# Optimization experiments

Hardware: AMD Instinct MI355X
Metric: run time of the kernel (lower is better)

## Reference

```python
import jax, jax.numpy as jnp
import numpy as np

LN_EPS = 1e-5
NUM_HEAD = 8


def _layernorm(x, gamma, beta):
    mu = jnp.mean(x, axis=-1, keepdims=True)
    var = jnp.var(x, axis=-1, keepdims=True)
    return (x - mu) * jax.lax.rsqrt(var + LN_EPS) * gamma + beta


def setup_inputs() -> dict:
    key = jax.random.key(0)
    ks = jax.random.split(key, 5)
    b, T, N, C = 16, 256, 24, 512
    scale = 1.0 / np.sqrt(C)
    return {
        "x": jax.random.normal(ks[0], (b, T, N, C), dtype=jnp.float32),
        "cross_x": jax.random.normal(ks[1], (b, T, N, C), dtype=jnp.float32),
        "gamma": jnp.ones((C,), dtype=jnp.float32),
        "beta": jnp.zeros((C,), dtype=jnp.float32),
        "Wq": (jax.random.normal(ks[2], (C, C), dtype=jnp.float32) * scale),
        "Wk": (jax.random.normal(ks[3], (C, C), dtype=jnp.float32) * scale),
        "Wv": (jax.random.normal(ks[4], (C, C), dtype=jnp.float32) * scale),
    }


def reference(x, cross_x, gamma, beta, Wq, Wk, Wv):
    b, T, N, C = x.shape
    H = NUM_HEAD
    d = C // H
    # fold joints into batch: (b, T, N, C) -> (b*N, T, C)
    xr = jnp.transpose(x, (0, 2, 1, 3)).reshape(b * N, T, C)
    cr = jnp.transpose(cross_x, (0, 2, 1, 3)).reshape(b * N, T, C)
    B = b * N
    xn = _layernorm(xr, gamma, beta)
    cn = _layernorm(cr, gamma, beta)
    # nn.Linear: y = x @ W.T (weight stored [out, in])
    q = jnp.einsum('btc,oc->bto', xn, Wq).reshape(B, T, H, d)
    k = jnp.einsum('btc,oc->bto', cn, Wk).reshape(B, T, H, d)
    v = jnp.einsum('btc,oc->bto', cn, Wv).reshape(B, T, H, d)
    att = jnp.einsum('bnhd,bmhd->bnmh', q, k) / np.sqrt(d).astype(np.float32)
    w = jax.nn.softmax(att, axis=2)  # softmax over key axis m (dropout=0)
    y = jnp.einsum('bnmh,bmhd->bnhd', w, v).reshape(B, T, C)
    y = xr + y
    return jnp.transpose(y.reshape(b, N, T, C), (0, 2, 1, 3))
```

## Files before the change

### kernel.cpp

```cpp
#include <hip/hip_runtime.h>

typedef __bf16 bf16x8 __attribute__((ext_vector_type(8)));
typedef float f32x4 __attribute__((ext_vector_type(4)));

#define MFMA16(a, b, c) __builtin_amdgcn_mfma_f32_16x16x32_bf16(a, b, c, 0, 0, 0)

__device__ __forceinline__ void gload_lds16(const void* g, void* l) {
  __builtin_amdgcn_global_load_lds(
      (const __attribute__((address_space(1))) void*)(unsigned long long)g,
      (__attribute__((address_space(3))) void*)(unsigned int)(unsigned long long)l,
      16, 0, 0);
}

__global__ void cvt_w_kernel(const float* __restrict__ wq, const float* __restrict__ wk,
                             const float* __restrict__ wv, __bf16* __restrict__ w) {
  int i = blockIdx.x * 256 + threadIdx.x;
  w[i]          = (__bf16)wq[i];
  w[i + 262144] = (__bf16)wk[i];
  w[i + 524288] = (__bf16)wv[i];
}

__global__ __launch_bounds__(256) void ln_kernel(
    const float* __restrict__ x, const float* __restrict__ cx,
    const float* __restrict__ g, const float* __restrict__ bet,
    __bf16* __restrict__ xn) {
  int wave = threadIdx.x >> 6, lane = threadIdx.x & 63;
  long row = (long)blockIdx.x * 4 + wave;
  const float* src = (row < 98304) ? (x + row * 512) : (cx + (row - 98304) * 512);
  const f32x4* p = (const f32x4*)(src + lane * 8);
  f32x4 a = p[0], b = p[1];
  float s  = a[0] + a[1] + a[2] + a[3] + b[0] + b[1] + b[2] + b[3];
  float s2 = a[0]*a[0] + a[1]*a[1] + a[2]*a[2] + a[3]*a[3]
           + b[0]*b[0] + b[1]*b[1] + b[2]*b[2] + b[3]*b[3];
  for (int d = 1; d < 64; d <<= 1) { s += __shfl_xor(s, d, 64); s2 += __shfl_xor(s2, d, 64); }
  float mean = s * (1.0f / 512.0f);
  float var  = s2 * (1.0f / 512.0f) - mean * mean;
  float rs = rsqrtf(var + 1e-5f);
  const f32x4* gp = (const f32x4*)(g + lane * 8);
  const f32x4* bp = (const f32x4*)(bet + lane * 8);
  f32x4 g0 = gp[0], g1 = gp[1], b0 = bp[0], b1 = bp[1];
  bf16x8 o;
  for (int j = 0; j < 4; ++j) o[j]     = (__bf16)((a[j] - mean) * rs * g0[j] + b0[j]);
  for (int j = 0; j < 4; ++j) o[4 + j] = (__bf16)((b[j] - mean) * rs * g1[j] + b1[j]);
  *(bf16x8*)(xn + row * 512 + lane * 8) = o;
}

__global__ __launch_bounds__(256) void gemm_qkv_kernel(
    const __bf16* __restrict__ act, const __bf16* __restrict__ w,
    __bf16* __restrict__ outqkv) {
  int z = blockIdx.z;
  const __bf16* A = act + (z ? (long)50331648 : 0);
  const __bf16* B = w + (long)z * 262144;
  __bf16* C = outqkv + (long)z * 50331648;
  int m0 = blockIdx.x * 128, n0 = blockIdx.y * 128;
  int tid = threadIdx.x, wave = tid >> 6, lane = tid & 63;
  int q4 = lane >> 4, cl = lane & 15;
  int wm = wave & 1, wn = wave >> 1;
  __shared__ __bf16 As[128 * 64];
  __shared__ __bf16 Bs[128 * 64];
  f32x4 acc[4][4] = {};
  for (int kb = 0; kb < 512; kb += 64) {
    for (int i = 0; i < 4; ++i) {
      int t = i * 256 + tid;
      int row = t >> 3;
      int col = (t & 7) * 8;
      gload_lds16(A + (long)(m0 + row) * 512 + kb + col, (char*)As + (i * 256 + wave * 64) * 16);
      gload_lds16(B + (long)(n0 + row) * 512 + kb + col, (char*)Bs + (i * 256 + wave * 64) * 16);
    }
    __syncthreads();
    for (int kc = 0; kc < 2; ++kc) {
      bf16x8 af[4], bfr[4];
      for (int mt = 0; mt < 4; ++mt)
        af[mt] = *(const bf16x8*)(As + (wm * 64 + mt * 16 + cl) * 64 + kc * 32 + q4 * 8);
      for (int nt = 0; nt < 4; ++nt)
        bfr[nt] = *(const bf16x8*)(Bs + (wn * 64 + nt * 16 + cl) * 64 + kc * 32 + q4 * 8);
      for (int mt = 0; mt < 4; ++mt)
        for (int nt = 0; nt < 4; ++nt)
          acc[mt][nt] = MFMA16(af[mt], bfr[nt], acc[mt][nt]);
    }
    __syncthreads();
  }
  for (int mt = 0; mt < 4; ++mt)
    for (int nt = 0; nt < 4; ++nt) {
      int row = m0 + wm * 64 + mt * 16 + q4 * 4;
      int col = n0 + wn * 64 + nt * 16 + cl;
      for (int r = 0; r < 4; ++r)
        C[(long)(row + r) * 512 + col] = (__bf16)acc[mt][nt][r];
    }
}

__global__ __launch_bounds__(256) void attn_kernel(
    const __bf16* __restrict__ Q, const __bf16* __restrict__ K,
    const __bf16* __restrict__ V, const float* __restrict__ x,
    float* __restrict__ out) {
  int blk = blockIdx.x;
  int h = blk & 7;
  int rem = blk >> 3;
  int n_ = rem % 24;
  int b_ = rem / 24;
  long base = ((long)b_ * 6144 + n_) * 512 + h * 64;
  const long ST = 12288;
  int tid = threadIdx.x, wave = tid >> 6, lane = tid & 63;
  int q4 = lane >> 4, cl = lane & 15;
  __shared__ __bf16 Vt[64][264];
  __shared__ __bf16 Pb[4][16][72];

  {
    const __bf16* vrow = V + base + (long)tid * ST;
    for (int i = 0; i < 8; ++i) {
      bf16x8 v = *(const bf16x8*)(vrow + i * 8);
      for (int j = 0; j < 8; ++j) Vt[i * 8 + j][tid] = v[j];
    }
  }
  __syncthreads();

  for (int iter = 0; iter < 4; ++iter) {
    int mt = iter * 4 + wave;
    int tq = mt * 16;
    const __bf16* qrow = Q + base + (long)(tq + cl) * ST;
    bf16x8 qa0 = *(const bf16x8*)(qrow + q4 * 8);
    bf16x8 qa1 = *(const bf16x8*)(qrow + 32 + q4 * 8);
    f32x4 s[16];
    for (int nt = 0; nt < 16; ++nt) {
      const __bf16* krow = K + base + (long)(nt * 16 + cl) * ST;
      bf16x8 kb0 = *(const bf16x8*)(krow + q4 * 8);
      bf16x8 kb1 = *(const bf16x8*)(krow + 32 + q4 * 8);
      f32x4 a = {};
      a = MFMA16(qa0, kb0, a);
      a = MFMA16(qa1, kb1, a);
      s[nt] = a;
    }
    float mx[4], l[4];
    for (int r = 0; r < 4; ++r) {
      float m = -1e30f;
      for (int nt = 0; nt < 16; ++nt) m = fmaxf(m, s[nt][r]);
      for (int d = 1; d < 16; d <<= 1) m = fmaxf(m, __shfl_xor(m, d, 64));
      mx[r] = m;
    }
    for (int r = 0; r < 4; ++r) l[r] = 0.0f;
    const float c_exp = 0.125f * 1.44269504088896f;
    for (int nt = 0; nt < 16; ++nt)
      for (int r = 0; r < 4; ++r) {
        float p = exp2f((s[nt][r] - mx[r]) * c_exp);
        s[nt][r] = p;
        l[r] += p;
      }
    for (int r = 0; r < 4; ++r)
      for (int d = 1; d < 16; d <<= 1) l[r] += __shfl_xor(l[r], d, 64);

    f32x4 o[4] = {};
    for (int ch = 0; ch < 4; ++ch) {
      for (int j = 0; j < 4; ++j)
        for (int r = 0; r < 4; ++r)
          Pb[wave][q4 * 4 + r][j * 16 + cl] = (__bf16)s[ch * 4 + j][r];
      __syncthreads();
      bf16x8 pa0 = *(const bf16x8*)(&Pb[wave][cl][0] + q4 * 8);
      bf16x8 pa1 = *(const bf16x8*)(&Pb[wave][cl][0] + 32 + q4 * 8);
      for (int dt = 0; dt < 4; ++dt) {
        bf16x8 vb0 = *(const bf16x8*)(&Vt[dt * 16 + cl][ch * 64] + q4 * 8);
        bf16x8 vb1 = *(const bf16x8*)(&Vt[dt * 16 + cl][ch * 64] + 32 + q4 * 8);
        o[dt] = MFMA16(pa0, vb0, o[dt]);
        o[dt] = MFMA16(pa1, vb1, o[dt]);
      }
      __syncthreads();
    }
    for (int dt = 0; dt < 4; ++dt)
      for (int r = 0; r < 4; ++r) {
        long addr = base + (long)(tq + q4 * 4 + r) * ST + dt * 16 + cl;
        out[addr] = x[addr] + o[dt][r] / l[r];
      }
  }
}

extern "C" void kernel_launch(void* const* d_in, const int* in_sizes, int n_in,
                              void* d_out, int out_size, void* d_ws, size_t ws_size,
                              hipStream_t stream) {
  const float* x     = (const float*)d_in[0];
  const float* cx    = (const float*)d_in[1];
  const float* gamma = (const float*)d_in[2];
  const float* beta  = (const float*)d_in[3];
  const float* Wq    = (const float*)d_in[4];
  const float* Wk    = (const float*)d_in[5];
  const float* Wv    = (const float*)d_in[6];
  float* out = (float*)d_out;
  char* ws = (char*)d_ws;

  __bf16* Wb = (__bf16*)(ws);
  __bf16* xn = (__bf16*)(ws + 1572864);
  __bf16* Qb = (__bf16*)(ws + 202899456);
  __bf16* Kb = (__bf16*)(ws + 303562752);
  __bf16* Vb = (__bf16*)(ws + 404226048);

  cvt_w_kernel<<<1024, 256, 0, stream>>>(Wq, Wk, Wv, Wb);
  ln_kernel<<<49152, 256, 0, stream>>>(x, cx, gamma, beta, xn);
  gemm_qkv_kernel<<<dim3(768, 4, 3), 256, 0, stream>>>(xn, Wb, Qb);
  attn_kernel<<<3072, 256, 0, stream>>>(Qb, Kb, Vb, x, out);
}
```

Baseline: 1.041 ms.

## Store Q/K/V head-contiguous and stage K/V in swizzled LDS for attention

The layernorm output is now written in (b,n,t) row order and the QKV GEMM epilogue scatters results into a per-(batch,joint,head) contiguous [256x64] layout, so the attention kernel reads contiguous 32KB tiles instead of rows strided by 12288 elements. The attention kernel loads K into XOR-swizzled LDS via direct global-to-LDS loads and transposes V into a swizzled buffer. It computes S^T so the probabilities stay in registers as MFMA operands, which removes the per-chunk LDS round trip for P and its block-wide barriers. The costs are a scattered, uncoalesced bf16 store pattern in the GEMM epilogue and extra index arithmetic in the layernorm.

```diff
diff --git a/kernel.cpp b/kernel.cpp
--- a/kernel.cpp
+++ b/kernel.cpp
@@ -26,7 +26,8 @@
     __bf16* __restrict__ xn) {
   int wave = threadIdx.x >> 6, lane = threadIdx.x & 63;
   long row = (long)blockIdx.x * 4 + wave;
-  const float* src = (row < 98304) ? (x + row * 512) : (cx + (row - 98304) * 512);
+  int rloc = (row < 98304) ? (int)row : (int)(row - 98304);
+  const float* src = (row < 98304) ? (x + row * 512) : (cx + (long)rloc * 512);
   const f32x4* p = (const f32x4*)(src + lane * 8);
   f32x4 a = p[0], b = p[1];
   float s  = a[0] + a[1] + a[2] + a[3] + b[0] + b[1] + b[2] + b[3];
@@ -42,7 +43,12 @@
   bf16x8 o;
   for (int j = 0; j < 4; ++j) o[j]     = (__bf16)((a[j] - mean) * rs * g0[j] + b0[j]);
   for (int j = 0; j < 4; ++j) o[4 + j] = (__bf16)((b[j] - mean) * rs * g1[j] + b1[j]);
-  *(bf16x8*)(xn + row * 512 + lane * 8) = o;
+  int b_ = rloc / 6144;
+  int rem = rloc - b_ * 6144;
+  int t_ = rem / 24;
+  int n_ = rem - t_ * 24;
+  long drow = (long)(b_ * 24 + n_) * 256 + t_ + ((row < 98304) ? 0 : 98304);
+  *(bf16x8*)(xn + drow * 512 + lane * 8) = o;
 }
 
 __global__ __launch_bounds__(256) void gemm_qkv_kernel(
@@ -82,10 +88,14 @@
   }
   for (int mt = 0; mt < 4; ++mt)
     for (int nt = 0; nt < 4; ++nt) {
-      int row = m0 + wm * 64 + mt * 16 + q4 * 4;
       int col = n0 + wn * 64 + nt * 16 + cl;
-      for (int r = 0; r < 4; ++r)
-        C[(long)(row + r) * 512 + col] = (__bf16)acc[mt][nt][r];
+      int hh = col >> 6, dd = col & 63;
+      int mbase = m0 + wm * 64 + mt * 16 + q4 * 4;
+      for (int r = 0; r < 4; ++r) {
+        int m = mbase + r;
+        long addr = ((long)((m >> 8) * 8 + hh) << 14) + ((m & 255) << 6) + dd;
+        C[addr] = (__bf16)acc[mt][nt][r];
+      }
     }
 }
 
@@ -95,80 +105,108 @@
     float* __restrict__ out) {
   int blk = blockIdx.x;
   int h = blk & 7;
-  int rem = blk >> 3;
-  int n_ = rem % 24;
-  int b_ = rem / 24;
-  long base = ((long)b_ * 6144 + n_) * 512 + h * 64;
-  const long ST = 12288;
+  int bn = blk >> 3;
+  int n_ = bn % 24;
+  int b_ = bn / 24;
+  const __bf16* Qh = Q + (long)blk * 16384;
+  const __bf16* Kh = K + (long)blk * 16384;
+  const __bf16* Vh = V + (long)blk * 16384;
+  long xbase = (long)b_ * 3145728 + (long)n_ * 512 + h * 64;
+
   int tid = threadIdx.x, wave = tid >> 6, lane = tid & 63;
   int q4 = lane >> 4, cl = lane & 15;
-  __shared__ __bf16 Vt[64][264];
-  __shared__ __bf16 Pb[4][16][72];
+
+  __shared__ __bf16 Ks[256 * 64];
+  __shared__ __bf16 Vt[64 * 256];
 
   {
-    const __bf16* vrow = V + base + (long)tid * ST;
+    int c = lane & 7;
+    int r8 = lane >> 3;
+    for (int it = 0; it < 8; ++it) {
+      int row = wave * 64 + it * 8 + r8;
+      gload_lds16(Kh + row * 64 + ((c ^ (row & 7)) << 3),
+                  (char*)Ks + (wave * 64 + it * 8) * 128);
+    }
+  }
+  {
+    int key = tid;
+    int colp = (key & ~31) | ((key & 12) << 1) | ((key & 16) >> 2) | (key & 3);
+    const __bf16* vrow = Vh + key * 64;
     for (int i = 0; i < 8; ++i) {
       bf16x8 v = *(const bf16x8*)(vrow + i * 8);
-      for (int j = 0; j < 8; ++j) Vt[i * 8 + j][tid] = v[j];
+      for (int j = 0; j < 8; ++j) {
+        int d = i * 8 + j;
+        *(__bf16*)((char*)Vt + d * 512 + ((colp * 2) ^ ((d & 7) << 4))) = v[j];
+      }
     }
   }
   __syncthreads();
 
+  const float c_exp = 0.125f * 1.44269504088896f;
   for (int iter = 0; iter < 4; ++iter) {
-    int mt = iter * 4 + wave;
-    int tq = mt * 16;
-    const __bf16* qrow = Q + base + (long)(tq + cl) * ST;
-    bf16x8 qa0 = *(const bf16x8*)(qrow + q4 * 8);
-    bf16x8 qa1 = *(const bf16x8*)(qrow + 32 + q4 * 8);
+    int qt = wave * 4 + iter;
+    const __bf16* qrow = Qh + (qt * 16 + cl) * 64 + q4 * 8;
+    bf16x8 qb0 = *(const bf16x8*)(qrow);
+    bf16x8 qb1 = *(const bf16x8*)(qrow + 32);
     f32x4 s[16];
-    for (int nt = 0; nt < 16; ++nt) {
-      const __bf16* krow = K + base + (long)(nt * 16 + cl) * ST;
-      bf16x8 kb0 = *(const bf16x8*)(krow + q4 * 8);
-      bf16x8 kb1 = *(const bf16x8*)(krow + 32 + q4 * 8);
+#pragma unroll
+    for (int kt = 0; kt < 16; ++kt) {
+      int row = kt * 16 + cl;
+      const char* kb = (const char*)Ks + row * 128;
+      bf16x8 ka0 = *(const bf16x8*)(kb + ((q4 ^ (row & 7)) << 4));
+      bf16x8 ka1 = *(const bf16x8*)(kb + (((4 + q4) ^ (row & 7)) << 4));
       f32x4 a = {};
-      a = MFMA16(qa0, kb0, a);
-      a = MFMA16(qa1, kb1, a);
-      s[nt] = a;
-    }
-    float mx[4], l[4];
+      a = MFMA16(ka0, qb0, a);
+      a = MFMA16(ka1, qb1, a);
+      s[kt] = a;
+    }
+    float mx = -1e30f;
+#pragma unroll
+    for (int kt = 0; kt < 16; ++kt)
+#pragma unroll
+      for (int r = 0; r < 4; ++r) mx = fmaxf(mx, s[kt][r]);
+    mx = fmaxf(mx, __shfl_xor(mx, 16, 64));
+    mx = fmaxf(mx, __shfl_xor(mx, 32, 64));
+    float lsum = 0.0f;
+#pragma unroll
+    for (int kt = 0; kt < 16; ++kt)
+#pragma unroll
+      for (int r = 0; r < 4; ++r) {
+        float p = exp2f((s[kt][r] - mx) * c_exp);
+        s[kt][r] = p;
+        lsum += p;
+      }
+    lsum += __shfl_xor(lsum, 16, 64);
+    lsum += __shfl_xor(lsum, 32, 64);
+
+    f32x4 o[4] = {};
+#pragma unroll
+    for (int m = 0; m < 8; ++m) {
+      bf16x8 pa;
+#pragma unroll
+      for (int j = 0; j < 4; ++j) {
+        pa[j]     = (__bf16)s[2 * m][j];
+        pa[4 + j] = (__bf16)s[2 * m + 1][j];
+      }
+#pragma unroll
+      for (int db = 0; db < 4; ++db) {
+        int row = db * 16 + cl;
+        bf16x8 vb = *(const bf16x8*)((const char*)Vt + row * 512 +
+                                     (((m * 4 + q4) ^ (row & 7)) << 4));
+        o[db] = MFMA16(pa, vb, o[db]);
+      }
+    }
+#pragma unroll
     for (int r = 0; r < 4; ++r) {
-      float m = -1e30f;
-      for (int nt = 0; nt < 16; ++nt) m = fmaxf(m, s[nt][r]);
-      for (int d = 1; d < 16; d <<= 1) m = fmaxf(m, __shfl_xor(m, d, 64));
-      mx[r] = m;
-    }
-    for (int r = 0; r < 4; ++r) l[r] = 0.0f;
-    const float c_exp = 0.125f * 1.44269504088896f;
-    for (int nt = 0; nt < 16; ++nt)
-      for (int r = 0; r < 4; ++r) {
-        float p = exp2f((s[nt][r] - mx[r]) * c_exp);
-        s[nt][r] = p;
-        l[r] += p;
-      }
-    for (int r = 0; r < 4; ++r)
-      for (int d = 1; d < 16; d <<= 1) l[r] += __shfl_xor(l[r], d, 64);
-
-    f32x4 o[4] = {};
-    for (int ch = 0; ch < 4; ++ch) {
-      for (int j = 0; j < 4; ++j)
-        for (int r = 0; r < 4; ++r)
-          Pb[wave][q4 * 4 + r][j * 16 + cl] = (__bf16)s[ch * 4 + j][r];
-      __syncthreads();
-      bf16x8 pa0 = *(const bf16x8*)(&Pb[wave][cl][0] + q4 * 8);
-      bf16x8 pa1 = *(const bf16x8*)(&Pb[wave][cl][0] + 32 + q4 * 8);
-      for (int dt = 0; dt < 4; ++dt) {
-        bf16x8 vb0 = *(const bf16x8*)(&Vt[dt * 16 + cl][ch * 64] + q4 * 8);
-        bf16x8 vb1 = *(const bf16x8*)(&Vt[dt * 16 + cl][ch * 64] + 32 + q4 * 8);
-        o[dt] = MFMA16(pa0, vb0, o[dt]);
-        o[dt] = MFMA16(pa1, vb1, o[dt]);
-      }
-      __syncthreads();
-    }
-    for (int dt = 0; dt < 4; ++dt)
-      for (int r = 0; r < 4; ++r) {
-        long addr = base + (long)(tq + q4 * 4 + r) * ST + dt * 16 + cl;
-        out[addr] = x[addr] + o[dt][r] / l[r];
-      }
+      float lr = __shfl(lsum, q4 * 4 + r, 64);
+      float inv = 1.0f / lr;
+      long trow = xbase + (long)(qt * 16 + q4 * 4 + r) * 12288;
+#pragma unroll
+      for (int db = 0; db < 4; ++db) {
+        long addr = trow + db * 16 + cl;
+        out[addr] = x[addr] + o[db][r] * inv;
+      }
+    }
   }
 }
 
@@ -188,11 +226,9 @@
   __bf16* Wb = (__bf16*)(ws);
   __bf16* xn = (__bf16*)(ws + 1572864);
   __bf16* Qb = (__bf16*)(ws + 202899456);
-  __bf16* Kb = (__bf16*)(ws + 303562752);
-  __bf16* Vb = (__bf16*)(ws + 404226048);
 
   cvt_w_kernel<<<1024, 256, 0, stream>>>(Wq, Wk, Wv, Wb);
   ln_kernel<<<49152, 256, 0, stream>>>(x, cx, gamma, beta, xn);
   gemm_qkv_kernel<<<dim3(768, 4, 3), 256, 0, stream>>>(xn, Wb, Qb);
-  attn_kernel<<<3072, 256, 0, stream>>>(Qb, Kb, Vb, x, out);
-}
+  attn_kernel<<<3072, 256, 0, stream>>>(Qb, Qb + 50331648, Qb + 100663296, x, out);
+}
```

Result: slower. 1.161 ms (+11.5%).
